# Kernel optimization log

Measured on AMD Instinct MI355X. Metric: run time of the kernel, lower is better.

## Reference

```python
import jax, jax.numpy as jnp
import numpy as np

VOCAB = 32000
D = 128          # dim_model == dim_embed
H = 8            # heads
DK = D // H
DFF = 512
NL = 4           # layers
NCLS = 10
N = 131072       # total tree nodes
NLEAF = 65536
ERAND = 524288   # random tree edges; self-loops appended -> E = ERAND + N
NREAD = 4096
MAXPOS = 2048


def _pe_table():
    # standard sinusoidal positional encoding table [MAXPOS, D]
    p = jnp.arange(MAXPOS, dtype=jnp.float32)[:, None]
    div = jnp.exp(jnp.arange(0, D, 2, dtype=jnp.float32) * (-np.log(10000.0) / D))
    ang = p * div
    pe = jnp.zeros((MAXPOS, D), jnp.float32)
    pe = pe.at[:, 0::2].set(jnp.sin(ang)).at[:, 1::2].set(jnp.cos(ang))
    return pe


def _ln(x, g, b, eps=1e-5):
    m = jnp.mean(x, axis=-1, keepdims=True)
    v = jnp.mean(jnp.square(x - m), axis=-1, keepdims=True)
    return (x - m) * jax.lax.rsqrt(v + eps) * g + b


def setup_inputs() -> dict:
    key = jax.random.key(0)
    ks = jax.random.split(key, 32)
    s = 1.0 / np.sqrt(D)
    inp = {}
    # graph / token inputs
    inp['x'] = jax.random.randint(ks[0], (NLEAF,), 0, VOCAB)
    inp['pos'] = jax.random.randint(ks[1], (NLEAF,), 0, MAXPOS)
    inp['leaf_ids'] = jnp.arange(NLEAF)
    src = jax.random.randint(ks[2], (ERAND,), 0, N)
    dst = jax.random.randint(ks[3], (ERAND,), 0, N)
    loops = jnp.arange(N)  # self loops so every node has >=1 incoming edge
    inp['src'] = jnp.concatenate([src, loops])
    inp['dst'] = jnp.concatenate([dst, loops])
    inp['readout_ids'] = jax.random.randint(ks[4], (NREAD,), 0, N)
    inp['h0'] = jnp.zeros((N, D), jnp.float32)  # internal nodes start at zero
    # parameters
    inp['embed_table'] = jax.random.normal(ks[5], (VOCAB, D)) * 0.02
    inp['emb_ng'] = jnp.ones((D,)); inp['emb_nb'] = jnp.zeros((D,))
    inp['Wq'] = jax.random.normal(ks[6], (NL, D, D)) * s
    inp['bq'] = jnp.zeros((NL, D))
    inp['Wk'] = jax.random.normal(ks[7], (NL, D, D)) * s
    inp['bk'] = jnp.zeros((NL, D))
    inp['Wv'] = jax.random.normal(ks[8], (NL, D, D)) * s
    inp['bv'] = jnp.zeros((NL, D))
    inp['Wo'] = jax.random.normal(ks[9], (NL, D, D)) * s
    inp['bo'] = jnp.zeros((NL, D))
    inp['ln1_g'] = jnp.ones((NL, D)); inp['ln1_b'] = jnp.zeros((NL, D))
    inp['W1'] = jax.random.normal(ks[10], (NL, D, DFF)) * s
    inp['b1'] = jnp.zeros((NL, DFF))
    inp['W2'] = jax.random.normal(ks[11], (NL, DFF, D)) * (1.0 / np.sqrt(DFF))
    inp['b2'] = jnp.zeros((NL, D))
    inp['ln2_g'] = jnp.ones((NL, D)); inp['ln2_b'] = jnp.zeros((NL, D))
    inp['gen_W'] = jax.random.normal(ks[12], (D, NCLS)) * s
    inp['gen_b'] = jnp.zeros((NCLS,))
    return inp


def reference(embed_table, emb_ng, emb_nb, Wq, bq, Wk, bk, Wv, bv, Wo, bo,
              ln1_g, ln1_b, W1, b1, W2, b2, ln2_g, ln2_b, gen_W, gen_b,
              h0, x, pos, leaf_ids, src, dst, readout_ids):
    pe = _pe_table()
    # leaf embedding (scaled, since rel_pos=False) + positional encoding, then LayerNorm
    hl = embed_table[x] * jnp.sqrt(jnp.float32(D)) + pe[pos]
    hl = _ln(hl, emb_ng, emb_nb)
    h = h0.at[leaf_ids].set(hl)  # [N, D]
    inv = 1.0 / np.sqrt(DK)
    for i in range(NL):
        q = (h @ Wq[i] + bq[i]).reshape(N, H, DK)
        k = (h @ Wk[i] + bk[i]).reshape(N, H, DK)
        v = (h @ Wv[i] + bv[i]).reshape(N, H, DK)
        # per-edge scaled dot-product scores [E, H]
        score = jnp.einsum('ehd,ehd->eh', q[dst], k[src]) * inv
        m = jax.lax.stop_gradient(jax.ops.segment_max(score, dst, num_segments=N))
        ex = jnp.exp(score - m[dst])
        den = jax.ops.segment_sum(ex, dst, num_segments=N)  # [N, H]
        agg = jax.ops.segment_sum(ex[:, :, None] * v[src], dst, num_segments=N)
        agg = agg / den[:, :, None]  # [N, H, DK]
        o = agg.reshape(N, D) @ Wo[i] + bo[i]
        h = _ln(h + o, ln1_g[i], ln1_b[i])
        ff = jax.nn.relu(h @ W1[i] + b1[i]) @ W2[i] + b2[i]
        h = _ln(h + ff, ln2_g[i], ln2_b[i])
    hr = h[readout_ids]
    return jax.nn.log_softmax(hr @ gen_W + gen_b, axis=-1)
```

## Files before the change

kernel.cpp:

```cpp
#include <hip/hip_runtime.h>
#include <hip/hip_bf16.h>

#define D 128
#define DFF 512
#define NLAYER 4
#define NCLS 10
#define NN 131072
#define NLEAF 65536
#define ETOT 655360
#define NREAD 4096

typedef unsigned short u16;
typedef unsigned int u32;
typedef __attribute__((ext_vector_type(8))) short bf16x8;
typedef __attribute__((ext_vector_type(16))) float f32x16;
typedef u32 u32x4 __attribute__((ext_vector_type(4)));

#define MFMA32(a,b,c) __builtin_amdgcn_mfma_f32_32x32x16_bf16(a,b,c,0,0,0)

__device__ __forceinline__ float b2f(u16 u){ u32 x = ((u32)u)<<16; return __builtin_bit_cast(float, x); }
__device__ __forceinline__ u16 f2b(float f){ u32 i = __builtin_bit_cast(u32, f); u32 r = (i + 0x7FFFu + ((i>>16)&1u))>>16; return (u16)r; }
__device__ __forceinline__ float blo(u32 u){ return __builtin_bit_cast(float, u<<16); }
__device__ __forceinline__ float bhi(u32 u){ return __builtin_bit_cast(float, u & 0xffff0000u); }

__device__ __forceinline__ float wredsum(float v){
  v += __shfl_xor(v,32); v += __shfl_xor(v,16); v += __shfl_xor(v,8);
  v += __shfl_xor(v,4);  v += __shfl_xor(v,2);  v += __shfl_xor(v,1);
  return v;
}
__device__ __forceinline__ float rsum32(float v){
  v += __shfl_xor(v,1); v += __shfl_xor(v,2); v += __shfl_xor(v,4);
  v += __shfl_xor(v,8); v += __shfl_xor(v,16);
  return v;
}

__device__ __forceinline__ bf16x8 ldfrag(const u16* buf, int row, int kbyte){
  return *(const bf16x8*)((const char*)buf + row*256 + ((u32)kbyte ^ (u32)((row&7)<<4)));
}

__device__ __forceinline__ void stage_B(const u16* __restrict__ src, int strideElems, int colOff,
                                        u16* BsBase, int wv_, int lane){
  int rb = wv_*32 + (lane>>4);
  int slotbase = lane & 15;
  #pragma unroll
  for(int it=0; it<8; it++){
    int r = rb + it*4;
    int slot = slotbase ^ (r&7);
    __builtin_amdgcn_global_load_lds(
      (const __attribute__((address_space(1))) unsigned*)(src + (size_t)r*strideElems + colOff + slot*8),
      (__attribute__((address_space(3))) unsigned*)((char*)BsBase + wv_*8192 + it*1024),
      16, 0, 0);
  }
}

__device__ __forceinline__ void mfma_regA(const bf16x8 af[8], const u16* Bs,
                                          int l31, int lkh, f32x16 acc[4]){
  #pragma unroll
  for(int kk=0;kk<8;kk++){
    #pragma unroll
    for(int c=0;c<4;c++){
      bf16x8 bf = ldfrag(Bs, c*32 + l31, kk*32 + lkh);
      acc[c] = MFMA32(af[kk], bf, acc[c]);
    }
  }
}

__device__ __forceinline__ void ln_epilogue(f32x16 acc[4], size_t r0, int wrow0, int l31, int h5,
    const float* g, const float* b, u16* hb){
  float gc[4], bc[4];
  #pragma unroll
  for(int c=0;c<4;c++){ int col = c*32 + l31; gc[c]=g[col]; bc[c]=b[col]; }
  #pragma unroll
  for(int r=0;r<16;r++){
    int rowl = wrow0 + (r&3) + 8*(r>>2) + 4*h5;
    size_t base = (r0 + rowl)*(size_t)D;
    float v[4];
    #pragma unroll
    for(int c=0;c<4;c++) v[c] = acc[c][r] + b2f(hb[base + c*32 + l31]);
    float s = rsum32(v[0]+v[1]+v[2]+v[3]);
    float mean = s * (1.0f/128.0f);
    float dd[4]; float q = 0.f;
    #pragma unroll
    for(int c=0;c<4;c++){ dd[c]=v[c]-mean; q += dd[c]*dd[c]; }
    q = rsum32(q);
    float rs = rsqrtf(q*(1.0f/128.0f) + 1e-5f);
    #pragma unroll
    for(int c=0;c<4;c++){
      float o = dd[c]*rs*gc[c] + bc[c];
      hb[base + c*32 + l31] = f2b(o);
    }
  }
}

__global__ __launch_bounds__(256) void k_hinit(const float* __restrict__ h0, u16* __restrict__ hb){
  int i = blockIdx.x*256 + threadIdx.x;
  float4 v = ((const float4*)h0)[i];
  ushort4 p; p.x=f2b(v.x); p.y=f2b(v.y); p.z=f2b(v.z); p.w=f2b(v.w);
  ((ushort4*)hb)[i] = p;
}

__global__ __launch_bounds__(256) void k_embed(const int* __restrict__ x, const int* __restrict__ pos,
    const int* __restrict__ leaf, const float* __restrict__ emb,
    const float* __restrict__ g, const float* __restrict__ b, u16* __restrict__ hb){
  int row = blockIdx.x*4 + (threadIdx.x>>6);
  int lane = threadIdx.x & 63;
  int tok = x[row]; float p = (float)pos[row];
  float v[2];
  #pragma unroll
  for(int j=0;j<2;j++){
    int d = lane + 64*j;
    float freq = expf(-0.07195578515529633f * (float)(d & ~1));
    float ang = p * freq;
    float pe = (d&1) ? cosf(ang) : sinf(ang);
    v[j] = emb[(size_t)tok*D + d] * 11.313708498984761f + pe;
  }
  float mean = wredsum(v[0]+v[1]) * (1.0f/128.0f);
  float d0 = v[0]-mean, d1 = v[1]-mean;
  float var = wredsum(d0*d0 + d1*d1) * (1.0f/128.0f);
  float rs = rsqrtf(var + 1e-5f);
  size_t orow = (size_t)leaf[row];
  hb[orow*D + lane]      = f2b(d0*rs*g[lane]    + b[lane]);
  hb[orow*D + lane + 64] = f2b(d1*rs*g[lane+64] + b[lane+64]);
}

__global__ __launch_bounds__(256) void k_wconv(const float* __restrict__ Wq, const float* __restrict__ Wk,
    const float* __restrict__ Wv, const float* __restrict__ Wo,
    const float* __restrict__ W1, const float* __restrict__ W2,
    u16* __restrict__ wqt, u16* __restrict__ wkt, u16* __restrict__ wvt, u16* __restrict__ wot,
    u16* __restrict__ w1t, u16* __restrict__ w2t){
  int e = blockIdx.x*256 + threadIdx.x;
  int l = e / 196608, r = e % 196608;
  if(r < 65536){
    int w = r >> 14, i = r & 16383;
    int n = i >> 7, k = i & 127;
    const float* src = (w==0)?Wq:(w==1)?Wk:(w==2)?Wv:Wo;
    u16* dst = (w==0)?wqt:(w==1)?wkt:(w==2)?wvt:wot;
    dst[l*16384 + n*128 + k] = f2b(src[l*16384 + k*128 + n]);
  } else if(r < 131072){
    int i = r - 65536; int n = i >> 7, k = i & 127;
    w1t[l*65536 + n*128 + k] = f2b(W1[l*65536 + k*512 + n]);
  } else {
    int i = r - 131072; int n = i >> 9, f = i & 511;
    w2t[l*65536 + n*512 + f] = f2b(W2[l*65536 + f*128 + n]);
  }
}

__global__ __launch_bounds__(256) void k_count(const int* __restrict__ dst, int* __restrict__ cnt){
  int e = blockIdx.x*256 + threadIdx.x;
  atomicAdd(&cnt[dst[e]], 1);
}
__global__ __launch_bounds__(256) void k_scan1(const int* __restrict__ cnt, int* __restrict__ part,
                                               int* __restrict__ bsum){
  __shared__ int s[256];
  int tid = threadIdx.x; int i = blockIdx.x*256 + tid;
  int v = cnt[i]; s[tid]=v; __syncthreads();
  for(int off=1; off<256; off<<=1){
    int t=(tid>=off)? s[tid-off]:0; __syncthreads();
    s[tid]+=t; __syncthreads();
  }
  part[i] = s[tid]-v;
  if(tid==255) bsum[blockIdx.x] = s[255];
}
__global__ __launch_bounds__(512) void k_scan2(int* __restrict__ bsum){
  __shared__ int s[512];
  int tid = threadIdx.x;
  int v = bsum[tid]; s[tid] = v; __syncthreads();
  for(int off=1; off<512; off<<=1){
    int t = (tid>=off)? s[tid-off]:0; __syncthreads();
    s[tid] += t; __syncthreads();
  }
  bsum[tid] = s[tid] - v;
}
__global__ __launch_bounds__(256) void k_scan3(const int* __restrict__ part, const int* __restrict__ bsum,
                                               int* __restrict__ indptr, int* __restrict__ cursor){
  int i = blockIdx.x*256 + threadIdx.x;
  int v = part[i] + bsum[i>>8];
  indptr[i] = v; cursor[i] = v;
  if(i==0) indptr[NN] = ETOT;
}
__global__ __launch_bounds__(256) void k_scatter(const int* __restrict__ src, const int* __restrict__ dst,
    int* __restrict__ cursor, int* __restrict__ esrc){
  int e = blockIdx.x*256 + threadIdx.x;
  int p = atomicAdd(&cursor[dst[e]], 1);
  esrc[p] = src[e];
}

__global__ __launch_bounds__(256,2) void k_qkv(const u16* __restrict__ hb,
    const u16* __restrict__ wqt, const u16* __restrict__ wkt, const u16* __restrict__ wvt,
    const float* __restrict__ bq, const float* __restrict__ bk, const float* __restrict__ bv,
    u16* __restrict__ qb, u16* __restrict__ kb, u16* __restrict__ vb){
  __shared__ u16 Bs[128*128];
  int tid = threadIdx.x;
  int lane = tid & 63, wv_ = tid >> 6;
  int l31 = lane & 31, h5 = lane >> 5, lkh = h5*16;
  int wrow0 = wv_*32;
  size_t r0 = (size_t)blockIdx.x * 128;
  int widx = blockIdx.y;
  const u16* wt = (widx==0)?wqt:(widx==1)?wkt:wvt;
  const float* bias = (widx==0)?bq:(widx==1)?bk:bv;
  u16* op = (widx==0)?qb:(widx==1)?kb:vb;

  stage_B(wt, D, 0, Bs, wv_, lane);
  bf16x8 af[8];
  const u16* arow = hb + (r0 + wrow0 + l31)*(size_t)D + h5*8;
  #pragma unroll
  for(int kk=0;kk<8;kk++) af[kk] = *(const bf16x8*)(arow + kk*16);

  f32x16 acc[4];
  #pragma unroll
  for(int c=0;c<4;c++){
    float bb = bias[c*32+l31];
    #pragma unroll
    for(int i=0;i<16;i++) acc[c][i] = bb;
  }
  __syncthreads();
  mfma_regA(af, Bs, l31, lkh, acc);
  #pragma unroll
  for(int c=0;c<4;c++){
    int col = c*32 + l31;
    #pragma unroll
    for(int r=0;r<16;r++){
      int row = wrow0 + (r&3) + 8*(r>>2) + 4*h5;
      op[(r0+row)*(size_t)D + col] = f2b(acc[c][r]);
    }
  }
}

__global__ __launch_bounds__(256,6) void k_attn(const u16* qb, const u16* __restrict__ kb,
    const u16* __restrict__ vb, const int* __restrict__ indptr, const int* __restrict__ esrc,
    u16* aggb){
  int node = blockIdx.x*4 + (threadIdx.x>>6);
  int lane = threadIdx.x & 63;
  int hd = lane >> 3, eslot = lane & 7;
  int beg = indptr[node], end = indptr[node+1];
  float qr[16];
  {
    const uint4* qp = (const uint4*)(qb + (size_t)node*D + hd*16);
    uint4 a = qp[0], b = qp[1];
    u32 w[8] = {a.x,a.y,a.z,a.w,b.x,b.y,b.z,b.w};
    #pragma unroll
    for(int i=0;i<8;i++){ qr[2*i] = blo(w[i]); qr[2*i+1] = bhi(w[i]); }
  }
  float m = -3.0e38f, den = 0.f;
  float acc[16];
  #pragma unroll
  for(int i=0;i<16;i++) acc[i] = 0.f;
  for(int e0=beg; e0<end; e0+=8){
    int e = e0 + eslot;
    if(e < end){
      int s = esrc[e];
      const uint4* kp = (const uint4*)(kb + (size_t)s*D + hd*16);
      uint4 k0 = kp[0], k1 = kp[1];
      const uint4* vp = (const uint4*)(vb + (size_t)s*D + hd*16);
      uint4 v0 = vp[0], v1 = vp[1];
      u32 kw[8] = {k0.x,k0.y,k0.z,k0.w,k1.x,k1.y,k1.z,k1.w};
      float p = 0.f, p2 = 0.f;
      #pragma unroll
      for(int i=0;i<8;i++){ p = fmaf(blo(kw[i]), qr[2*i], p); p2 = fmaf(bhi(kw[i]), qr[2*i+1], p2); }
      p = (p + p2)*0.25f;
      float nm = fmaxf(m, p);
      float fs = __expf(m - nm);
      float w  = __expf(p - nm);
      den = den*fs + w;
      u32 vw[8] = {v0.x,v0.y,v0.z,v0.w,v1.x,v1.y,v1.z,v1.w};
      #pragma unroll
      for(int i=0;i<8;i++){
        acc[2*i]   = fmaf(acc[2*i],   fs, w*blo(vw[i]));
        acc[2*i+1] = fmaf(acc[2*i+1], fs, w*bhi(vw[i]));
      }
      m = nm;
    }
  }
  float mo = m;
  #pragma unroll
  for(int s=1; s<8; s<<=1){
    float m2 = __shfl_xor(m, s); float d2 = __shfl_xor(den, s);
    float nm = fmaxf(m, m2);
    den = den*__expf(m-nm) + d2*__expf(m2-nm);
    m = nm;
  }
  float sc = __expf(mo - m);
  #pragma unroll
  for(int i=0;i<16;i++) acc[i] *= sc;
  #pragma unroll
  for(int lvl=0; lvl<3; lvl++){
    const int half = 8 >> lvl;
    const int msk = 4 >> lvl;
    bool hi = (eslot & msk) != 0;
    #pragma unroll
    for(int i=0;i<half;i++){
      float a = acc[i], b = acc[i+half];
      acc[i]      = hi ? b : a;
      acc[i+half] = hi ? a : b;
    }
    #pragma unroll
    for(int i=0;i<half;i++) acc[i] += __shfl_xor(acc[i+half], msk);
  }
  float rin = 1.0f/den;
  u32 pk = (u32)f2b(acc[0]*rin) | ((u32)f2b(acc[1]*rin)<<16);
  *(u32*)(aggb + (size_t)node*D + hd*16 + eslot*2) = pk;
}

__global__ __launch_bounds__(256,2) void k_owo(const u16* __restrict__ aggb, const u16* __restrict__ wot,
    const float* __restrict__ bo, const float* __restrict__ g1, const float* __restrict__ b1,
    u16* hb){
  __shared__ u16 Bs[128*128];
  int tid = threadIdx.x;
  int lane = tid & 63, wv_ = tid >> 6;
  int l31 = lane & 31, h5 = lane >> 5, lkh = h5*16;
  int wrow0 = wv_*32;
  size_t r0 = (size_t)blockIdx.x * 128;
  stage_B(wot, D, 0, Bs, wv_, lane);
  bf16x8 af[8];
  const u16* arow = aggb + (r0 + wrow0 + l31)*(size_t)D + h5*8;
  #pragma unroll
  for(int kk=0;kk<8;kk++) af[kk] = *(const bf16x8*)(arow + kk*16);
  f32x16 acc[4];
  #pragma unroll
  for(int c=0;c<4;c++){
    float bb = bo[c*32+l31];
    #pragma unroll
    for(int i=0;i<16;i++) acc[c][i] = bb;
  }
  __syncthreads();
  mfma_regA(af, Bs, l31, lkh, acc);
  ln_epilogue(acc, r0, wrow0, l31, h5, g1, b1, hb);
}

__global__ __launch_bounds__(256,2) void k_ffn(const u16* __restrict__ w1t, const u16* __restrict__ w2t,
    const float* __restrict__ b1, const float* __restrict__ b2,
    const float* __restrict__ g2, const float* __restrict__ bb2,
    u16* hb){
  __shared__ u16 B1s[128*128];
  __shared__ u16 B2s[128*128];
  int tid = threadIdx.x;
  int lane = tid & 63, wv_ = tid >> 6;
  int l31 = lane & 31, h5 = lane >> 5, lkh = h5*16;
  int wrow0 = wv_*32;
  size_t r0 = (size_t)blockIdx.x * 128;
  bf16x8 af[8];
  const u16* arow = hb + (r0 + wrow0 + l31)*(size_t)D + h5*8;
  #pragma unroll
  for(int kk=0;kk<8;kk++) af[kk] = *(const bf16x8*)(arow + kk*16);
  f32x16 out[4];
  #pragma unroll
  for(int c=0;c<4;c++){
    float bb = b2[c*32+l31];
    #pragma unroll
    for(int i=0;i<16;i++) out[c][i] = bb;
  }
  for(int ch=0; ch<4; ch++){
    if(ch) __syncthreads();
    stage_B(w1t + ch*128*D, D, 0, B1s, wv_, lane);
    stage_B(w2t, DFF, ch*128, B2s, wv_, lane);
    __syncthreads();
    f32x16 acc2[4];
    #pragma unroll
    for(int c=0;c<4;c++){
      #pragma unroll
      for(int r=0;r<16;r++){
        int foff = (r&3) + 8*(r>>2) + 4*h5;
        acc2[c][r] = b1[ch*128 + c*32 + foff];
      }
    }
    #pragma unroll
    for(int kk=0;kk<8;kk++){
      #pragma unroll
      for(int c=0;c<4;c++){
        bf16x8 w1f = ldfrag(B1s, c*32 + l31, kk*32 + lkh);
        acc2[c] = MFMA32(w1f, af[kk], acc2[c]);
      }
    }
    bf16x8 af2[8];
    bool hb5 = (h5 != 0);
    #pragma unroll
    for(int c=0;c<4;c++){
      u32 pk[8];
      #pragma unroll
      for(int t=0;t<8;t++){
        float lo  = fmaxf(acc2[c][2*t],   0.f);
        float hi2 = fmaxf(acc2[c][2*t+1], 0.f);
        u32 r_;
        asm("v_cvt_pk_bf16_f32 %0, %1, %2" : "=v"(r_) : "v"(lo), "v"(hi2));
        pk[t] = r_;
      }
      u32 s0 = hb5 ? pk[0] : pk[2];
      u32 s1 = hb5 ? pk[1] : pk[3];
      u32 s2 = hb5 ? pk[4] : pk[6];
      u32 s3 = hb5 ? pk[5] : pk[7];
      u32 g0 = (u32)__shfl_xor((int)s0, 32);
      u32 g1 = (u32)__shfl_xor((int)s1, 32);
      u32 g2_ = (u32)__shfl_xor((int)s2, 32);
      u32 g3 = (u32)__shfl_xor((int)s3, 32);
      u32x4 A0 = { hb5 ? g0 : pk[0], hb5 ? g1 : pk[1], hb5 ? pk[2] : g0, hb5 ? pk[3] : g1 };
      u32x4 A1 = { hb5 ? g2_ : pk[4], hb5 ? g3 : pk[5], hb5 ? pk[6] : g2_, hb5 ? pk[7] : g3 };
      af2[2*c]   = __builtin_bit_cast(bf16x8, A0);
      af2[2*c+1] = __builtin_bit_cast(bf16x8, A1);
    }
    #pragma unroll
    for(int kk=0;kk<8;kk++){
      #pragma unroll
      for(int c=0;c<4;c++){
        bf16x8 w2f = ldfrag(B2s, c*32 + l31, kk*32 + lkh);
        out[c] = MFMA32(af2[kk], w2f, out[c]);
      }
    }
  }
  ln_epilogue(out, r0, wrow0, l31, h5, g2, bb2, hb);
}

__global__ __launch_bounds__(64) void k_readout(const u16* __restrict__ hb, const int* __restrict__ rid,
    const float* __restrict__ gw, const float* __restrict__ gb, float* __restrict__ out){
  int r = blockIdx.x; int lane = threadIdx.x;
  size_t node = (size_t)rid[r];
  float h0v = b2f(hb[node*D + lane]), h1v = b2f(hb[node*D + 64 + lane]);
  float lg[NCLS];
  #pragma unroll
  for(int c=0;c<NCLS;c++){
    float p = h0v*gw[lane*NCLS + c] + h1v*gw[(lane+64)*NCLS + c];
    lg[c] = wredsum(p) + gb[c];
  }
  float mx = lg[0];
  #pragma unroll
  for(int c=1;c<NCLS;c++) mx = fmaxf(mx, lg[c]);
  float se = 0.f;
  #pragma unroll
  for(int c=0;c<NCLS;c++) se += expf(lg[c]-mx);
  float lse = mx + logf(se);
  if(lane < NCLS) out[(size_t)r*NCLS + lane] = lg[lane] - lse;
}

extern "C" void kernel_launch(void* const* d_in, const int* in_sizes, int n_in,
                              void* d_out, int out_size, void* d_ws, size_t ws_size,
                              hipStream_t stream) {
  const int* x    = (const int*)d_in[0];
  const int* pos  = (const int*)d_in[1];
  const int* leaf = (const int*)d_in[2];
  const int* src  = (const int*)d_in[3];
  const int* dst  = (const int*)d_in[4];
  const int* rid  = (const int*)d_in[5];
  const float* h0 = (const float*)d_in[6];
  const float* emb= (const float*)d_in[7];
  const float* eng= (const float*)d_in[8];
  const float* enb= (const float*)d_in[9];
  const float* Wq = (const float*)d_in[10];
  const float* bq = (const float*)d_in[11];
  const float* Wk = (const float*)d_in[12];
  const float* bk = (const float*)d_in[13];
  const float* Wv = (const float*)d_in[14];
  const float* bv = (const float*)d_in[15];
  const float* Wo = (const float*)d_in[16];
  const float* bo = (const float*)d_in[17];
  const float* l1g= (const float*)d_in[18];
  const float* l1b= (const float*)d_in[19];
  const float* W1 = (const float*)d_in[20];
  const float* b1 = (const float*)d_in[21];
  const float* W2 = (const float*)d_in[22];
  const float* b2 = (const float*)d_in[23];
  const float* l2g= (const float*)d_in[24];
  const float* l2b= (const float*)d_in[25];
  const float* gw = (const float*)d_in[26];
  const float* gb = (const float*)d_in[27];
  float* out = (float*)d_out;

  char* ws = (char*)d_ws;
  u16* hb     = (u16*)(ws);
  u16* qb     = (u16*)(ws + 33554432);
  u16* kb     = (u16*)(ws + 67108864);
  u16* vb     = (u16*)(ws + 100663296);
  u16* wqt    = (u16*)(ws + 134217728);
  u16* wkt    = (u16*)(ws + 134348800);
  u16* wvt    = (u16*)(ws + 134479872);
  u16* wot    = (u16*)(ws + 134610944);
  u16* w1t    = (u16*)(ws + 134742016);
  u16* w2t    = (u16*)(ws + 135266304);
  int* indptr = (int*)(ws + 135790592);
  int* cursor = (int*)(ws + 136315136);
  int* part   = (int*)(ws + 136839424);
  int* bsum   = (int*)(ws + 137363712);
  int* esrc   = (int*)(ws + 137365760);

  k_hinit<<<NN*D/4/256, 256, 0, stream>>>(h0, hb);
  k_embed<<<NLEAF/4, 256, 0, stream>>>(x, pos, leaf, emb, eng, enb, hb);
  k_wconv<<<NLAYER*196608/256, 256, 0, stream>>>(Wq,Wk,Wv,Wo,W1,W2, wqt,wkt,wvt,wot,w1t,w2t);

  hipMemsetAsync(cursor, 0, NN*sizeof(int), stream);
  k_count  <<<ETOT/256, 256, 0, stream>>>(dst, cursor);
  k_scan1  <<<NN/256, 256, 0, stream>>>(cursor, part, bsum);
  k_scan2  <<<1, 512, 0, stream>>>(bsum);
  k_scan3  <<<NN/256, 256, 0, stream>>>(part, bsum, indptr, cursor);
  k_scatter<<<ETOT/256, 256, 0, stream>>>(src, dst, cursor, esrc);

  for(int l=0; l<NLAYER; l++){
    k_qkv<<<dim3(NN/128,3), 256, 0, stream>>>(hb, wqt + l*16384, wkt + l*16384, wvt + l*16384,
                                              bq + l*D, bk + l*D, bv + l*D, qb, kb, vb);
    k_attn<<<NN/4, 256, 0, stream>>>(qb, kb, vb, indptr, esrc, qb);
    k_owo<<<NN/128, 256, 0, stream>>>(qb, wot + l*16384, bo + l*D,
                                      l1g + l*D, l1b + l*D, hb);
    k_ffn<<<NN/128, 256, 0, stream>>>(w1t + l*65536, w2t + l*65536,
                                      b1 + l*DFF, b2 + l*D, l2g + l*D, l2b + l*D, hb);
  }
  k_readout<<<NREAD, 64, 0, stream>>>(hb, rid, gw, gb, out);
}
```

Before: 842.1 us.

## Fuse output projection with FFN and compute Q/K/V in one block

The O-projection plus LN1 kernel and the FFN plus LN2 kernel become one kernel. The post-LN1 hidden state stays in swizzled LDS, so it is no longer written to global memory and read back. The QKV kernel now loads the A tile once and loops over the three weight matrices in a single block instead of using a 3-wide grid. The cost is more barriers and serialized weight staging into one shared buffer (W1 and W2 are now staged one after the other), and fewer blocks in the QKV grid.

```diff
diff --git a/kernel.cpp b/kernel.cpp
--- a/kernel.cpp
+++ b/kernel.cpp
@@ -61,33 +61,6 @@
     for(int c=0;c<4;c++){
       bf16x8 bf = ldfrag(Bs, c*32 + l31, kk*32 + lkh);
       acc[c] = MFMA32(af[kk], bf, acc[c]);
-    }
-  }
-}
-
-__device__ __forceinline__ void ln_epilogue(f32x16 acc[4], size_t r0, int wrow0, int l31, int h5,
-    const float* g, const float* b, u16* hb){
-  float gc[4], bc[4];
-  #pragma unroll
-  for(int c=0;c<4;c++){ int col = c*32 + l31; gc[c]=g[col]; bc[c]=b[col]; }
-  #pragma unroll
-  for(int r=0;r<16;r++){
-    int rowl = wrow0 + (r&3) + 8*(r>>2) + 4*h5;
-    size_t base = (r0 + rowl)*(size_t)D;
-    float v[4];
-    #pragma unroll
-    for(int c=0;c<4;c++) v[c] = acc[c][r] + b2f(hb[base + c*32 + l31]);
-    float s = rsum32(v[0]+v[1]+v[2]+v[3]);
-    float mean = s * (1.0f/128.0f);
-    float dd[4]; float q = 0.f;
-    #pragma unroll
-    for(int c=0;c<4;c++){ dd[c]=v[c]-mean; q += dd[c]*dd[c]; }
-    q = rsum32(q);
-    float rs = rsqrtf(q*(1.0f/128.0f) + 1e-5f);
-    #pragma unroll
-    for(int c=0;c<4;c++){
-      float o = dd[c]*rs*gc[c] + bc[c];
-      hb[base + c*32 + l31] = f2b(o);
     }
   }
 }
@@ -195,33 +168,40 @@
   int l31 = lane & 31, h5 = lane >> 5, lkh = h5*16;
   int wrow0 = wv_*32;
   size_t r0 = (size_t)blockIdx.x * 128;
-  int widx = blockIdx.y;
-  const u16* wt = (widx==0)?wqt:(widx==1)?wkt:wvt;
-  const float* bias = (widx==0)?bq:(widx==1)?bk:bv;
-  u16* op = (widx==0)?qb:(widx==1)?kb:vb;
-
-  stage_B(wt, D, 0, Bs, wv_, lane);
+
+  stage_B(wqt, D, 0, Bs, wv_, lane);
   bf16x8 af[8];
   const u16* arow = hb + (r0 + wrow0 + l31)*(size_t)D + h5*8;
   #pragma unroll
   for(int kk=0;kk<8;kk++) af[kk] = *(const bf16x8*)(arow + kk*16);
 
-  f32x16 acc[4];
-  #pragma unroll
-  for(int c=0;c<4;c++){
-    float bb = bias[c*32+l31];
-    #pragma unroll
-    for(int i=0;i<16;i++) acc[c][i] = bb;
-  }
-  __syncthreads();
-  mfma_regA(af, Bs, l31, lkh, acc);
-  #pragma unroll
-  for(int c=0;c<4;c++){
-    int col = c*32 + l31;
-    #pragma unroll
-    for(int r=0;r<16;r++){
-      int row = wrow0 + (r&3) + 8*(r>>2) + 4*h5;
-      op[(r0+row)*(size_t)D + col] = f2b(acc[c][r]);
+  const u16* wt[3]    = {wqt,wkt,wvt};
+  const float* bias[3] = {bq,bk,bv};
+  u16* outp[3] = {qb,kb,vb};
+  #pragma unroll
+  for(int w=0; w<3; w++){
+    if(w){
+      __syncthreads();
+      stage_B(wt[w], D, 0, Bs, wv_, lane);
+    }
+    f32x16 acc[4];
+    #pragma unroll
+    for(int c=0;c<4;c++){
+      float bb = bias[w][c*32+l31];
+      #pragma unroll
+      for(int i=0;i<16;i++) acc[c][i] = bb;
+    }
+    __syncthreads();
+    mfma_regA(af, Bs, l31, lkh, acc);
+    u16* op = outp[w];
+    #pragma unroll
+    for(int c=0;c<4;c++){
+      int col = c*32 + l31;
+      #pragma unroll
+      for(int r=0;r<16;r++){
+        int row = wrow0 + (r&3) + 8*(r>>2) + 4*h5;
+        op[(r0+row)*(size_t)D + col] = f2b(acc[c][r]);
+      }
     }
   }
 }
@@ -301,20 +281,28 @@
   *(u32*)(aggb + (size_t)node*D + hd*16 + eslot*2) = pk;
 }
 
-__global__ __launch_bounds__(256,2) void k_owo(const u16* __restrict__ aggb, const u16* __restrict__ wot,
-    const float* __restrict__ bo, const float* __restrict__ g1, const float* __restrict__ b1,
+__global__ __launch_bounds__(256,2) void k_owoffn(const u16* __restrict__ aggb,
+    const u16* __restrict__ wot, const float* __restrict__ bo,
+    const float* __restrict__ g1, const float* __restrict__ c1,
+    const u16* __restrict__ w1t, const u16* __restrict__ w2t,
+    const float* __restrict__ fb1, const float* __restrict__ fb2,
+    const float* __restrict__ g2, const float* __restrict__ c2,
     u16* hb){
   __shared__ u16 Bs[128*128];
+  __shared__ u16 Ts[128*128];
   int tid = threadIdx.x;
   int lane = tid & 63, wv_ = tid >> 6;
   int l31 = lane & 31, h5 = lane >> 5, lkh = h5*16;
   int wrow0 = wv_*32;
   size_t r0 = (size_t)blockIdx.x * 128;
+
   stage_B(wot, D, 0, Bs, wv_, lane);
   bf16x8 af[8];
-  const u16* arow = aggb + (r0 + wrow0 + l31)*(size_t)D + h5*8;
-  #pragma unroll
-  for(int kk=0;kk<8;kk++) af[kk] = *(const bf16x8*)(arow + kk*16);
+  {
+    const u16* arow = aggb + (r0 + wrow0 + l31)*(size_t)D + h5*8;
+    #pragma unroll
+    for(int kk=0;kk<8;kk++) af[kk] = *(const bf16x8*)(arow + kk*16);
+  }
   f32x16 acc[4];
   #pragma unroll
   for(int c=0;c<4;c++){
@@ -324,35 +312,48 @@
   }
   __syncthreads();
   mfma_regA(af, Bs, l31, lkh, acc);
-  ln_epilogue(acc, r0, wrow0, l31, h5, g1, b1, hb);
-}
-
-__global__ __launch_bounds__(256,2) void k_ffn(const u16* __restrict__ w1t, const u16* __restrict__ w2t,
-    const float* __restrict__ b1, const float* __restrict__ b2,
-    const float* __restrict__ g2, const float* __restrict__ bb2,
-    u16* hb){
-  __shared__ u16 B1s[128*128];
-  __shared__ u16 B2s[128*128];
-  int tid = threadIdx.x;
-  int lane = tid & 63, wv_ = tid >> 6;
-  int l31 = lane & 31, h5 = lane >> 5, lkh = h5*16;
-  int wrow0 = wv_*32;
-  size_t r0 = (size_t)blockIdx.x * 128;
-  bf16x8 af[8];
-  const u16* arow = hb + (r0 + wrow0 + l31)*(size_t)D + h5*8;
-  #pragma unroll
-  for(int kk=0;kk<8;kk++) af[kk] = *(const bf16x8*)(arow + kk*16);
+
+  {
+    float gc[4], bc[4];
+    #pragma unroll
+    for(int c=0;c<4;c++){ int col = c*32 + l31; gc[c]=g1[col]; bc[c]=c1[col]; }
+    #pragma unroll
+    for(int r=0;r<16;r++){
+      int rowl = wrow0 + (r&3) + 8*(r>>2) + 4*h5;
+      size_t base = (r0 + rowl)*(size_t)D;
+      float v[4];
+      #pragma unroll
+      for(int c=0;c<4;c++) v[c] = acc[c][r] + b2f(hb[base + c*32 + l31]);
+      float s = rsum32(v[0]+v[1]+v[2]+v[3]);
+      float mean = s * (1.0f/128.0f);
+      float dd[4]; float q = 0.f;
+      #pragma unroll
+      for(int c=0;c<4;c++){ dd[c]=v[c]-mean; q += dd[c]*dd[c]; }
+      q = rsum32(q);
+      float rs = rsqrtf(q*(1.0f/128.0f) + 1e-5f);
+      #pragma unroll
+      for(int c=0;c<4;c++){
+        int col = c*32 + l31;
+        float o = dd[c]*rs*gc[c] + bc[c];
+        *(u16*)((char*)Ts + rowl*256 + (u32)((col*2) ^ ((rowl&7)<<4))) = f2b(o);
+      }
+    }
+  }
+  __syncthreads();
+
+  bf16x8 afH[8];
+  #pragma unroll
+  for(int kk=0;kk<8;kk++) afH[kk] = ldfrag(Ts, wrow0 + l31, kk*32 + lkh);
+
   f32x16 out[4];
   #pragma unroll
   for(int c=0;c<4;c++){
-    float bb = b2[c*32+l31];
+    float bb = fb2[c*32+l31];
     #pragma unroll
     for(int i=0;i<16;i++) out[c][i] = bb;
   }
   for(int ch=0; ch<4; ch++){
-    if(ch) __syncthreads();
-    stage_B(w1t + ch*128*D, D, 0, B1s, wv_, lane);
-    stage_B(w2t, DFF, ch*128, B2s, wv_, lane);
+    stage_B(w1t + ch*128*D, D, 0, Bs, wv_, lane);
     __syncthreads();
     f32x16 acc2[4];
     #pragma unroll
@@ -360,15 +361,15 @@
       #pragma unroll
       for(int r=0;r<16;r++){
         int foff = (r&3) + 8*(r>>2) + 4*h5;
-        acc2[c][r] = b1[ch*128 + c*32 + foff];
+        acc2[c][r] = fb1[ch*128 + c*32 + foff];
       }
     }
     #pragma unroll
     for(int kk=0;kk<8;kk++){
       #pragma unroll
       for(int c=0;c<4;c++){
-        bf16x8 w1f = ldfrag(B1s, c*32 + l31, kk*32 + lkh);
-        acc2[c] = MFMA32(w1f, af[kk], acc2[c]);
+        bf16x8 w1f = ldfrag(Bs, c*32 + l31, kk*32 + lkh);
+        acc2[c] = MFMA32(w1f, afH[kk], acc2[c]);
       }
     }
     bf16x8 af2[8];
@@ -389,24 +390,57 @@
       u32 s2 = hb5 ? pk[4] : pk[6];
       u32 s3 = hb5 ? pk[5] : pk[7];
       u32 g0 = (u32)__shfl_xor((int)s0, 32);
-      u32 g1 = (u32)__shfl_xor((int)s1, 32);
+      u32 g1_ = (u32)__shfl_xor((int)s1, 32);
       u32 g2_ = (u32)__shfl_xor((int)s2, 32);
       u32 g3 = (u32)__shfl_xor((int)s3, 32);
-      u32x4 A0 = { hb5 ? g0 : pk[0], hb5 ? g1 : pk[1], hb5 ? pk[2] : g0, hb5 ? pk[3] : g1 };
+      u32x4 A0 = { hb5 ? g0 : pk[0], hb5 ? g1_ : pk[1], hb5 ? pk[2] : g0, hb5 ? pk[3] : g1_ };
       u32x4 A1 = { hb5 ? g2_ : pk[4], hb5 ? g3 : pk[5], hb5 ? pk[6] : g2_, hb5 ? pk[7] : g3 };
       af2[2*c]   = __builtin_bit_cast(bf16x8, A0);
       af2[2*c+1] = __builtin_bit_cast(bf16x8, A1);
     }
+    __syncthreads();
+    stage_B(w2t, DFF, ch*128, Bs, wv_, lane);
+    __syncthreads();
     #pragma unroll
     for(int kk=0;kk<8;kk++){
       #pragma unroll
       for(int c=0;c<4;c++){
-        bf16x8 w2f = ldfrag(B2s, c*32 + l31, kk*32 + lkh);
+        bf16x8 w2f = ldfrag(Bs, c*32 + l31, kk*32 + lkh);
         out[c] = MFMA32(af2[kk], w2f, out[c]);
       }
     }
-  }
-  ln_epilogue(out, r0, wrow0, l31, h5, g2, bb2, hb);
+    if(ch<3) __syncthreads();
+  }
+
+  {
+    float gc[4], bc[4];
+    #pragma unroll
+    for(int c=0;c<4;c++){ int col = c*32 + l31; gc[c]=g2[col]; bc[c]=c2[col]; }
+    #pragma unroll
+    for(int r=0;r<16;r++){
+      int rowl = wrow0 + (r&3) + 8*(r>>2) + 4*h5;
+      size_t base = (r0 + rowl)*(size_t)D;
+      float v[4];
+      #pragma unroll
+      for(int c=0;c<4;c++){
+        int col = c*32 + l31;
+        float res = b2f(*(const u16*)((const char*)Ts + rowl*256 + (u32)((col*2) ^ ((rowl&7)<<4))));
+        v[c] = out[c][r] + res;
+      }
+      float s = rsum32(v[0]+v[1]+v[2]+v[3]);
+      float mean = s * (1.0f/128.0f);
+      float dd[4]; float q = 0.f;
+      #pragma unroll
+      for(int c=0;c<4;c++){ dd[c]=v[c]-mean; q += dd[c]*dd[c]; }
+      q = rsum32(q);
+      float rs = rsqrtf(q*(1.0f/128.0f) + 1e-5f);
+      #pragma unroll
+      for(int c=0;c<4;c++){
+        float o = dd[c]*rs*gc[c] + bc[c];
+        hb[base + c*32 + l31] = f2b(o);
+      }
+    }
+  }
 }
 
 __global__ __launch_bounds__(64) void k_readout(const u16* __restrict__ hb, const int* __restrict__ rid,
@@ -492,13 +526,14 @@
   k_scatter<<<ETOT/256, 256, 0, stream>>>(src, dst, cursor, esrc);
 
   for(int l=0; l<NLAYER; l++){
-    k_qkv<<<dim3(NN/128,3), 256, 0, stream>>>(hb, wqt + l*16384, wkt + l*16384, wvt + l*16384,
-                                              bq + l*D, bk + l*D, bv + l*D, qb, kb, vb);
+    k_qkv<<<NN/128, 256, 0, stream>>>(hb, wqt + l*16384, wkt + l*16384, wvt + l*16384,
+                                      bq + l*D, bk + l*D, bv + l*D, qb, kb, vb);
     k_attn<<<NN/4, 256, 0, stream>>>(qb, kb, vb, indptr, esrc, qb);
-    k_owo<<<NN/128, 256, 0, stream>>>(qb, wot + l*16384, bo + l*D,
-                                      l1g + l*D, l1b + l*D, hb);
-    k_ffn<<<NN/128, 256, 0, stream>>>(w1t + l*65536, w2t + l*65536,
-                                      b1 + l*DFF, b2 + l*D, l2g + l*D, l2b + l*D, hb);
+    k_owoffn<<<NN/128, 256, 0, stream>>>(qb, wot + l*16384, bo + l*D,
+                                         l1g + l*D, l1b + l*D,
+                                         w1t + l*65536, w2t + l*65536,
+                                         b1 + l*DFF, b2 + l*D,
+                                         l2g + l*D, l2b + l*D, hb);
   }
   k_readout<<<NREAD, 64, 0, stream>>>(hb, rid, gw, gb, out);
 }
```

Measured after the change: 969.7 us. +15.2%, slower.
